# Performance work log

Hardware: AMD Instinct MI355X
Metric: run time of the kernel (lower is better)

Reference implementation:

```python
import jax, jax.numpy as jnp
import numpy as np

# CIM / quantization constants hardcoded in the source module
INPUT_BIT = 8
WEIGHT_BIT = 4
OUTPUT_BIT = 8
DAC_BIT = 2
ADC_BIT = 8
ADC_GAIN_1_SCALE = 1.0 / 63.0
GAIN_MIN, GAIN_MAX = 1.0, 255.0
N_SLICES = INPUT_BIT // DAC_BIT  # 4 bit-serial input slices of 2 bits each


def ste_round(v):
    # straight-through round: forward = round(v), backward = identity
    return v + jax.lax.stop_gradient(jnp.round(v) - v)


def conv2d(x, w):
    # NCHW conv, stride 1, padding k//2 (SAME for odd k)
    return jax.lax.conv_general_dilated(
        x, w, window_strides=(1, 1), padding='SAME',
        dimension_numbers=('NCHW', 'OIHW', 'NCHW'))


def setup_inputs() -> dict:
    key = jax.random.key(0)
    kx, kw, kb = jax.random.split(key, 3)
    B, Cin, H, W = 16, 4, 512, 512
    Cout, K = 8, 3
    x = jax.random.uniform(kx, (B, Cin, H, W), dtype=jnp.float32)  # non-negative activations
    weight = jax.random.normal(kw, (Cout, Cin, K, K), dtype=jnp.float32) * 0.05
    bias = jax.random.normal(kb, (Cout,), dtype=jnp.float32) * 0.01
    s_in = jnp.float32(1.0 / 255.0)   # LSQ input scale (8-bit unsigned)
    s_w = jnp.float32(0.02)           # LSQ weight scale (4-bit signed)
    s_out = jnp.float32(0.05)         # LSQ output scale (8-bit signed)
    return {"x": x, "weight": weight, "bias": bias,
            "s_in": s_in, "s_w": s_w, "s_out": s_out}


def reference(x, weight, bias, s_in, s_w, s_out):
    in_max = 2.0 ** INPUT_BIT - 1.0          # 255
    w_lim = 2.0 ** (WEIGHT_BIT - 1) - 1.0    # 7
    adc_max = 2.0 ** (ADC_BIT - 1) - 1.0     # 127
    o_lim = 2.0 ** (OUTPUT_BIT - 1) - 1.0    # 127
    base = float(2 ** DAC_BIT)               # 4 levels per DAC slice

    # LSQ quantization of input (unsigned) and weight (signed), STE rounding
    xq = jnp.clip(ste_round(x / s_in), 0.0, in_max)        # integer-valued floats
    wq = jnp.clip(ste_round(weight / s_w), -w_lim, w_lim)

    # ideal integer conv (gradient path)
    ideal = conv2d(xq, wq)

    # bit-serial DAC/ADC CIM path (forward only; noise_scale=0 so no noise)
    xi = jax.lax.stop_gradient(xq)
    wi = jax.lax.stop_gradient(wq)
    psums = []
    for s in range(N_SLICES):
        sl = jnp.mod(jnp.floor(xi / (base ** s)), base)    # 2-bit slice in [0,3]
        psums.append(conv2d(sl, wi))
    # ADC gain adjustment ('gain' mode): integer gain in [1,255], LSB = 1/(gain*gain_1_scale)
    p_absmax = jnp.maximum(
        jnp.max(jnp.stack([jnp.max(jnp.abs(p)) for p in psums])), 1e-6)
    gain = jnp.clip(jnp.round(adc_max / (p_absmax * ADC_GAIN_1_SCALE)),
                    GAIN_MIN, GAIN_MAX)
    step = 1.0 / (gain * ADC_GAIN_1_SCALE)
    acc = jnp.zeros_like(ideal)
    for s, p in enumerate(psums):
        adc_out = jnp.clip(jnp.round(p / step), -adc_max, adc_max) * step
        acc = acc + adc_out * (base ** s)

    # straight-through: forward uses analog path, backward uses ideal conv
    psum = ideal + jax.lax.stop_gradient(acc - ideal)

    out = psum * (s_in * s_w) + bias[None, :, None, None]
    # LSQ output quantization (8-bit signed)
    out = jnp.clip(ste_round(out / s_out), -o_lim, o_lim) * s_out
    return out
```

## Files before the change

kernel.cpp:

```cpp
#include <hip/hip_runtime.h>
#include <stdint.h>

#define B_   16
#define CIN  4
#define COUT 8
#define H_   512
#define W_   512
#define HP   (H_ + 2)
#define WP   (W_ + 2)
#define PMAX 756
#define TBL  (2 * PMAX + 1)
#define RPB  8
#define GY   (H_ / RPB)
#define NBLK (2 * GY * B_)
#define NQ   (B_ * HP)

__device__ __forceinline__ int dot4(uint32_t a, int b, int c) {
#if __has_builtin(__builtin_amdgcn_sdot4)
    return __builtin_amdgcn_sdot4((int)a, b, c, false);
#else
    int r = c;
#pragma unroll
    for (int i = 0; i < 4; ++i) {
        int av = (int)((a >> (8 * i)) & 0xFFu);
        int bv = ((int)(((uint32_t)b) << (24 - 8 * i))) >> 24;
        r += av * bv;
    }
    return r;
#endif
}

__device__ __forceinline__ int dot8(uint32_t a, int b, int c) {
#if __has_builtin(__builtin_amdgcn_sdot8)
    return __builtin_amdgcn_sdot8((int)a, b, c, false);
#else
    int r = c;
#pragma unroll
    for (int i = 0; i < 8; ++i) {
        int av = (int)((a >> (4 * i)) & 0xFu);
        int bv = ((int)(((uint32_t)b) << (28 - 4 * i))) >> 28;
        r += av * bv;
    }
    return r;
#endif
}

__device__ __forceinline__ float rfl_f(float v) {
    return __int_as_float(__builtin_amdgcn_readfirstlane(__float_as_int(v)));
}

__device__ __forceinline__ int wquant(const float* w, float s_w,
                                      int co, int ci, int tap) {
    const int kh = tap / 3, kw = tap % 3;
    float wv = w[((co * CIN + ci) * 3 + kh) * 3 + kw];
    float q  = rintf(__fdiv_rn(wv, s_w));
    q = fminf(fmaxf(q, -7.0f), 7.0f);
    return (int)q;
}

__global__ __launch_bounds__(128) void quant_pack_kernel(
        const float* __restrict__ x, const float* __restrict__ weight,
        const float* __restrict__ s_in_p, const float* __restrict__ s_w_p,
        uint32_t* __restrict__ xq, uint32_t* __restrict__ wq8) {
    const int raw = blockIdx.x;
    const int lin = (raw & 7) * (NQ / 8) + (raw >> 3);
    const int b = lin / HP, hp = lin % HP;
    const int t = threadIdx.x;
    if (raw == 0) {
        const float s_w = *s_w_p;
        if (t < 32) {
            const int co = t >> 2, p = t & 3;
            const int tA = (p == 0) ? 0 : (p == 1) ? 3 : (p == 2) ? 6 : 2;
            const int tB = (p == 0) ? 1 : (p == 1) ? 4 : (p == 2) ? 7 : 5;
            uint32_t v = 0;
#pragma unroll
            for (int ci = 0; ci < CIN; ++ci) {
                v |= ((uint32_t)(wquant(weight, s_w, co, ci, tA) & 0xF)) << (8 * ci);
                v |= ((uint32_t)(wquant(weight, s_w, co, ci, tB) & 0xF)) << (8 * ci + 4);
            }
            wq8[t] = v;
        } else if (t < 40) {
            const int co = t - 32;
            uint32_t v = 0;
#pragma unroll
            for (int ci = 0; ci < CIN; ++ci)
                v |= ((uint32_t)(wquant(weight, s_w, co, ci, 8) & 0xFF)) << (8 * ci);
            wq8[32 + co] = v;
        }
    }
    uint32_t* dst = xq + ((size_t)b * HP + hp) * WP;
    if (hp == 0 || hp == HP - 1) {
        for (int i = t; i < WP; i += 128) dst[i] = 0;
        return;
    }
    const float s_in = *s_in_p;
    const int h = hp - 1;
    const size_t plane = (size_t)H_ * W_;
    const float* xr = x + ((size_t)b * CIN) * plane + (size_t)h * W_ + 4 * t;
    float4 v0 = *(const float4*)(xr);
    float4 v1 = *(const float4*)(xr + plane);
    float4 v2 = *(const float4*)(xr + 2 * plane);
    float4 v3 = *(const float4*)(xr + 3 * plane);
    uint32_t o0 = 0, o1 = 0, o2 = 0, o3 = 0;
#define QP(f, ci, oj)                                                  \
    { float q = rintf(__fdiv_rn((f), s_in));                           \
      q = fminf(fmaxf(q, 0.0f), 255.0f);                               \
      oj |= ((uint32_t)(int)q) << (8 * (ci)); }
    QP(v0.x, 0, o0) QP(v0.y, 0, o1) QP(v0.z, 0, o2) QP(v0.w, 0, o3)
    QP(v1.x, 1, o0) QP(v1.y, 1, o1) QP(v1.z, 1, o2) QP(v1.w, 1, o3)
    QP(v2.x, 2, o0) QP(v2.y, 2, o1) QP(v2.z, 2, o2) QP(v2.w, 2, o3)
    QP(v3.x, 3, o0) QP(v3.y, 3, o1) QP(v3.z, 3, o2) QP(v3.w, 3, o3)
#undef QP
    uint32_t* d = dst + 1 + 4 * t;
    d[0] = o0; d[1] = o1; d[2] = o2; d[3] = o3;
    if (t == 0) dst[0] = 0;
    if (t == 127) dst[WP - 1] = 0;
}

#define LOADW()                                                              \
    int w8s[32], w4s[8];                                                     \
    {                                                                        \
        const int4* q4 = (const int4*)wq8;                                   \
        _Pragma("unroll")                                                    \
        for (int i = 0; i < 8; ++i) {                                        \
            int4 w4i = q4[i];                                                \
            w8s[4 * i + 0] = __builtin_amdgcn_readfirstlane(w4i.x);          \
            w8s[4 * i + 1] = __builtin_amdgcn_readfirstlane(w4i.y);          \
            w8s[4 * i + 2] = __builtin_amdgcn_readfirstlane(w4i.z);          \
            w8s[4 * i + 3] = __builtin_amdgcn_readfirstlane(w4i.w);          \
        }                                                                    \
        int4 a0 = q4[8], a1 = q4[9];                                         \
        w4s[0] = __builtin_amdgcn_readfirstlane(a0.x);                       \
        w4s[1] = __builtin_amdgcn_readfirstlane(a0.y);                       \
        w4s[2] = __builtin_amdgcn_readfirstlane(a0.z);                       \
        w4s[3] = __builtin_amdgcn_readfirstlane(a0.w);                       \
        w4s[4] = __builtin_amdgcn_readfirstlane(a1.x);                       \
        w4s[5] = __builtin_amdgcn_readfirstlane(a1.y);                       \
        w4s[6] = __builtin_amdgcn_readfirstlane(a1.z);                       \
        w4s[7] = __builtin_amdgcn_readfirstlane(a1.w);                       \
    }

#define SWZ()                                                                \
    const int raw = blockIdx.x;                                              \
    const int lin = (raw & 7) * (NBLK / 8) + (raw >> 3);                     \
    const int bx = lin & 1;                                                  \
    const int hy = (lin >> 1) & (GY - 1);                                    \
    const int b  = lin >> 7;                                                 \
    const int w0 = bx * 256 + threadIdx.x;                                   \
    const int h0 = hy * RPB;

#define EXTS(CA, SG, v0, v1, v2)                                             \
    do {                                                                     \
        uint32_t lo_ = ((v0) & 0x0F0F0F0Fu) | (((v1) << 4) & 0xF0F0F0F0u);   \
        uint32_t hi_ = (((v0) >> 4) & 0x0F0F0F0Fu) | ((v1) & 0xF0F0F0F0u);   \
        CA[0] = lo_ & 0x33333333u;                                           \
        CA[1] = (lo_ >> 2) & 0x33333333u;                                    \
        CA[2] = hi_ & 0x33333333u;                                           \
        CA[3] = (hi_ >> 2) & 0x33333333u;                                    \
        SG[0] = (v2)&0x03030303u;                                            \
        SG[1] = ((v2) >> 2) & 0x03030303u;                                   \
        SG[2] = ((v2) >> 4) & 0x03030303u;                                   \
        SG[3] = ((v2) >> 6) & 0x03030303u;                                   \
    } while (0)

#define RING_INIT()                                                          \
    uint32_t cA0[4], cA1[4], cA2[4], cA3[4];                                 \
    uint32_t sg0[4], sg1[4], sg2[4], sg3[4];                                 \
    {                                                                        \
        uint32_t r0 = base[0], r1 = base[1], r2 = base[2];                   \
        EXTS(cA0, sg0, r0, r1, r2);                                          \
        r0 = base[WP]; r1 = base[WP + 1]; r2 = base[WP + 2];                 \
        EXTS(cA1, sg1, r0, r1, r2);                                          \
    }                                                                        \
    uint32_t n0 = base[2 * WP], n1 = base[2 * WP + 1], n2 = base[2 * WP + 2];

#define PREF(S)                                                              \
    if ((S) < RPB - 1) {                                                     \
        const uint32_t* nr_ = base + (size_t)((S) + 3) * WP;                 \
        n0 = nr_[0]; n1 = nr_[1]; n2 = nr_[2];                               \
    }

#define DOTS(CAa, SGa, CAb, SGb, CAc, SGc, K, INIT, OUTV)                    \
    {                                                                        \
        int a_ = dot4(SGc[K], w4s[co], INIT);                                \
        a_ = dot8(CAa[K], w8s[co * 4 + 0], a_);                              \
        a_ = dot8(CAb[K], w8s[co * 4 + 1], a_);                              \
        a_ = dot8(CAc[K], w8s[co * 4 + 2], a_);                              \
        a_ = dot8(K == 0 ? pc0 : K == 1 ? pc1 : K == 2 ? pc2 : pc3,          \
                  w8s[co * 4 + 3], a_);                                      \
        OUTV = a_;                                                           \
    }

#define STEP1(S, CAa, SGa, CAb, SGb, CAc, SGc)                               \
    do {                                                                     \
        EXTS(CAc, SGc, n0, n1, n2);                                          \
        PREF(S);                                                             \
        const uint32_t pc0 = SGa[0] | (SGb[0] << 4);                         \
        const uint32_t pc1 = SGa[1] | (SGb[1] << 4);                         \
        const uint32_t pc2 = SGa[2] | (SGb[2] << 4);                         \
        const uint32_t pc3 = SGa[3] | (SGb[3] << 4);                         \
        _Pragma("unroll")                                                    \
        for (int co = 0; co < COUT; ++co) {                                  \
            int a0, a1, a2, a3;                                              \
            DOTS(CAa, SGa, CAb, SGb, CAc, SGc, 0, 0, a0);                    \
            DOTS(CAa, SGa, CAb, SGb, CAc, SGc, 1, 0, a1);                    \
            DOTS(CAa, SGa, CAb, SGb, CAc, SGc, 2, 0, a2);                    \
            DOTS(CAa, SGa, CAb, SGb, CAc, SGc, 3, 0, a3);                    \
            rMax0 = max(rMax0, a0); rMin0 = min(rMin0, a0);                  \
            rMax1 = max(rMax1, a1); rMin1 = min(rMin1, a1);                  \
            rMax2 = max(rMax2, a2); rMin2 = min(rMin2, a2);                  \
            rMax3 = max(rMax3, a3); rMin3 = min(rMin3, a3);                  \
        }                                                                    \
    } while (0)

__global__ __launch_bounds__(256, 8) void conv_absmax(
        const uint32_t* __restrict__ xq, const uint32_t* __restrict__ wq8,
        int* __restrict__ blkmax) {
    __shared__ int red[4];
    LOADW();
    SWZ();
    const uint32_t* base = xq + ((size_t)b * HP + h0) * WP + w0;
    RING_INIT();
    int rMax0 = 0, rMax1 = 0, rMax2 = 0, rMax3 = 0;
    int rMin0 = 0, rMin1 = 0, rMin2 = 0, rMin3 = 0;
    STEP1(0, cA0, sg0, cA1, sg1, cA2, sg2);
    STEP1(1, cA1, sg1, cA2, sg2, cA3, sg3);
    STEP1(2, cA2, sg2, cA3, sg3, cA0, sg0);
    STEP1(3, cA3, sg3, cA0, sg0, cA1, sg1);
    STEP1(4, cA0, sg0, cA1, sg1, cA2, sg2);
    STEP1(5, cA1, sg1, cA2, sg2, cA3, sg3);
    STEP1(6, cA2, sg2, cA3, sg3, cA0, sg0);
    STEP1(7, cA3, sg3, cA0, sg0, cA1, sg1);
    int m = max(max(max(rMax0, -rMin0), max(rMax1, -rMin1)),
                max(max(rMax2, -rMin2), max(rMax3, -rMin3)));
#pragma unroll
    for (int off = 1; off < 64; off <<= 1)
        m = max(m, __shfl_xor(m, off));
    if ((threadIdx.x & 63) == 0) red[threadIdx.x >> 6] = m;
    __syncthreads();
    if (threadIdx.x == 0)
        blkmax[raw] = max(max(red[0], red[1]), max(red[2], red[3]));
}

__global__ __launch_bounds__(256) void reduce_absmax(
        const int* __restrict__ blkmax, int* __restrict__ absmax) {
    __shared__ int red[4];
    const int t = threadIdx.x;
    int m = 0;
#pragma unroll
    for (int i = 0; i < NBLK / 256; ++i) m = max(m, blkmax[t + 256 * i]);
#pragma unroll
    for (int off = 1; off < 64; off <<= 1)
        m = max(m, __shfl_xor(m, off));
    if ((t & 63) == 0) red[t >> 6] = m;
    __syncthreads();
    if (t == 0)
        *absmax = max(max(red[0], red[1]), max(red[2], red[3]));
}

#define STEP2(S, CAa, SGa, CAb, SGb, CAc, SGc)                               \
    do {                                                                     \
        EXTS(CAc, SGc, n0, n1, n2);                                          \
        PREF(S);                                                             \
        const uint32_t pc0 = SGa[0] | (SGb[0] << 4);                         \
        const uint32_t pc1 = SGa[1] | (SGb[1] << 4);                         \
        const uint32_t pc2 = SGa[2] | (SGb[2] << 4);                         \
        const uint32_t pc3 = SGa[3] | (SGb[3] << 4);                         \
        float* orow = out + ((size_t)b * COUT * H_ + (size_t)(h0 + (S))) * W_ + w0; \
        _Pragma("unroll")                                                    \
        for (int co = 0; co < COUT; ++co) {                                  \
            int a0, a1, a2, a3;                                              \
            DOTS(CAa, SGa, CAb, SGb, CAc, SGc, 0, PMAX, a0);                 \
            DOTS(CAa, SGa, CAb, SGb, CAc, SGc, 1, PMAX, a1);                 \
            DOTS(CAa, SGa, CAb, SGb, CAc, SGc, 2, PMAX, a2);                 \
            DOTS(CAa, SGa, CAb, SGb, CAc, SGc, 3, PMAX, a3);                 \
            float of = tbl[a0];                                              \
            of = __fadd_rn(of, __fmul_rn(tbl[a1], 4.0f));                    \
            of = __fadd_rn(of, __fmul_rn(tbl[a2], 16.0f));                   \
            of = __fadd_rn(of, __fmul_rn(tbl[a3], 64.0f));                   \
            float o_ = __fadd_rn(__fmul_rn(of, scale), br[co]);              \
            float q_ = rintf(__fdiv_rn(o_, s_out));                          \
            q_ = fminf(fmaxf(q_, -127.0f), 127.0f);                          \
            orow[(size_t)co * plane] = __fmul_rn(q_, s_out);                 \
        }                                                                    \
    } while (0)

__global__ __launch_bounds__(256, 4) void conv_out(
        const uint32_t* __restrict__ xq, const uint32_t* __restrict__ wq8,
        const float* __restrict__ bias, const float* __restrict__ sp_in,
        const float* __restrict__ sp_w, const float* __restrict__ sp_out,
        const int* __restrict__ absmax, float* __restrict__ out) {
    __shared__ float tbl[TBL];
    LOADW();
    const float pabs = fmaxf((float)(*absmax), 1e-6f);
    const float c63  = 1.0f / 63.0f;
    float g = rintf(__fdiv_rn(127.0f, __fmul_rn(pabs, c63)));
    g = fminf(fmaxf(g, 1.0f), 255.0f);
    const float step = __fdiv_rn(1.0f, __fmul_rn(g, c63));
    for (int i = threadIdx.x; i < TBL; i += 256) {
        float p = (float)(i - PMAX);
        float r = rintf(__fdiv_rn(p, step));
        r = fminf(fmaxf(r, -127.0f), 127.0f);
        tbl[i] = __fmul_rn(r, step);
    }
    const float scale = __fmul_rn(rfl_f(*sp_in), rfl_f(*sp_w));
    const float s_out = rfl_f(*sp_out);
    float br[COUT];
#pragma unroll
    for (int co = 0; co < COUT; ++co) br[co] = rfl_f(bias[co]);
    __syncthreads();

    SWZ();
    const uint32_t* base = xq + ((size_t)b * HP + h0) * WP + w0;
    const size_t plane = (size_t)H_ * W_;
    RING_INIT();
    STEP2(0, cA0, sg0, cA1, sg1, cA2, sg2);
    STEP2(1, cA1, sg1, cA2, sg2, cA3, sg3);
    STEP2(2, cA2, sg2, cA3, sg3, cA0, sg0);
    STEP2(3, cA3, sg3, cA0, sg0, cA1, sg1);
    STEP2(4, cA0, sg0, cA1, sg1, cA2, sg2);
    STEP2(5, cA1, sg1, cA2, sg2, cA3, sg3);
    STEP2(6, cA2, sg2, cA3, sg3, cA0, sg0);
    STEP2(7, cA3, sg3, cA0, sg0, cA1, sg1);
}

extern "C" void kernel_launch(void* const* d_in, const int* in_sizes, int n_in,
                              void* d_out, int out_size, void* d_ws, size_t ws_size,
                              hipStream_t stream) {
    const float* x      = (const float*)d_in[0];
    const float* weight = (const float*)d_in[1];
    const float* bias   = (const float*)d_in[2];
    const float* s_in   = (const float*)d_in[3];
    const float* s_w    = (const float*)d_in[4];
    const float* s_out  = (const float*)d_in[5];
    float* out = (float*)d_out;

    int*      absmax = (int*)d_ws;
    uint32_t* wq8    = (uint32_t*)((char*)d_ws + 256);
    int*      blkmax = (int*)((char*)d_ws + 1024);
    uint32_t* xq     = (uint32_t*)((char*)d_ws + 16384);

    quant_pack_kernel<<<dim3(NQ), dim3(128), 0, stream>>>(
        x, weight, s_in, s_w, xq, wq8);

    conv_absmax<<<dim3(NBLK), dim3(256), 0, stream>>>(xq, wq8, blkmax);

    reduce_absmax<<<dim3(1), dim3(256), 0, stream>>>(blkmax, absmax);

    conv_out<<<dim3(NBLK), dim3(256), 0, stream>>>(
        xq, wq8, bias, s_in, s_w, s_out, absmax, out);
}
```

Baseline: 99.14 us.

## Replace ADC LUT and IEEE divides with reciprocal-based inline quantization

Removes the shared-memory ADC lookup table and its barrier, and computes each ADC quantization inline using a precomputed reciprocal of the step plus one Newton/FMA correction. The IEEE divides in input quantization and output quantization are replaced the same way, which removes the slow division sequences. The launch bound that asked for 4 blocks per SM is dropped, so the compiler has more freedom with registers. The risk is extra ALU work per output in place of LDS gathers, and rounding may differ from exact division in rare ties.

Measured after the change: 111.2 us. 1.12x slower.

```diff
diff --git a/kernel.cpp b/kernel.cpp
--- a/kernel.cpp
+++ b/kernel.cpp
@@ -9,7 +9,6 @@
 #define HP   (H_ + 2)
 #define WP   (W_ + 2)
 #define PMAX 756
-#define TBL  (2 * PMAX + 1)
 #define RPB  8
 #define GY   (H_ / RPB)
 #define NBLK (2 * GY * B_)
@@ -47,6 +46,24 @@
 
 __device__ __forceinline__ float rfl_f(float v) {
     return __int_as_float(__builtin_amdgcn_readfirstlane(__float_as_int(v)));
+}
+
+__device__ __forceinline__ float recip1(float d) {
+    float y0 = __builtin_amdgcn_rcpf(d);
+    float e  = fmaf(-d, y0, 1.0f);
+    return fmaf(y0, e, y0);
+}
+__device__ __forceinline__ float mdiv(float n, float d, float y) {
+    float q0 = __fmul_rn(n, y);
+    float rr = fmaf(-d, q0, n);
+    return fmaf(rr, y, q0);
+}
+
+__device__ __forceinline__ float adc1(int a, float step, float istep) {
+    float pf = (float)a;
+    float q  = rintf(mdiv(pf, step, istep));
+    q = fminf(fmaxf(q, -127.0f), 127.0f);
+    return __fmul_rn(q, step);
 }
 
 __device__ __forceinline__ int wquant(const float* w, float s_w,
@@ -94,6 +111,7 @@
         return;
     }
     const float s_in = *s_in_p;
+    const float yin  = recip1(s_in);
     const int h = hp - 1;
     const size_t plane = (size_t)H_ * W_;
     const float* xr = x + ((size_t)b * CIN) * plane + (size_t)h * W_ + 4 * t;
@@ -103,7 +121,7 @@
     float4 v3 = *(const float4*)(xr + 3 * plane);
     uint32_t o0 = 0, o1 = 0, o2 = 0, o3 = 0;
 #define QP(f, ci, oj)                                                  \
-    { float q = rintf(__fdiv_rn((f), s_in));                           \
+    { float q = rintf(mdiv((f), s_in, yin));                           \
       q = fminf(fmaxf(q, 0.0f), 255.0f);                               \
       oj |= ((uint32_t)(int)q) << (8 * (ci)); }
     QP(v0.x, 0, o0) QP(v0.y, 0, o1) QP(v0.z, 0, o2) QP(v0.w, 0, o3)
@@ -180,9 +198,9 @@
         n0 = nr_[0]; n1 = nr_[1]; n2 = nr_[2];                               \
     }
 
-#define DOTS(CAa, SGa, CAb, SGb, CAc, SGc, K, INIT, OUTV)                    \
+#define DOTS(CAa, SGa, CAb, SGb, CAc, SGc, K, OUTV)                          \
     {                                                                        \
-        int a_ = dot4(SGc[K], w4s[co], INIT);                                \
+        int a_ = dot4(SGc[K], w4s[co], 0);                                   \
         a_ = dot8(CAa[K], w8s[co * 4 + 0], a_);                              \
         a_ = dot8(CAb[K], w8s[co * 4 + 1], a_);                              \
         a_ = dot8(CAc[K], w8s[co * 4 + 2], a_);                              \
@@ -202,10 +220,10 @@
         _Pragma("unroll")                                                    \
         for (int co = 0; co < COUT; ++co) {                                  \
             int a0, a1, a2, a3;                                              \
-            DOTS(CAa, SGa, CAb, SGb, CAc, SGc, 0, 0, a0);                    \
-            DOTS(CAa, SGa, CAb, SGb, CAc, SGc, 1, 0, a1);                    \
-            DOTS(CAa, SGa, CAb, SGb, CAc, SGc, 2, 0, a2);                    \
-            DOTS(CAa, SGa, CAb, SGb, CAc, SGc, 3, 0, a3);                    \
+            DOTS(CAa, SGa, CAb, SGb, CAc, SGc, 0, a0);                       \
+            DOTS(CAa, SGa, CAb, SGb, CAc, SGc, 1, a1);                       \
+            DOTS(CAa, SGa, CAb, SGb, CAc, SGc, 2, a2);                       \
+            DOTS(CAa, SGa, CAb, SGb, CAc, SGc, 3, a3);                       \
             rMax0 = max(rMax0, a0); rMin0 = min(rMin0, a0);                  \
             rMax1 = max(rMax1, a1); rMin1 = min(rMin1, a1);                  \
             rMax2 = max(rMax2, a2); rMin2 = min(rMin2, a2);                  \
@@ -270,45 +288,42 @@
         _Pragma("unroll")                                                    \
         for (int co = 0; co < COUT; ++co) {                                  \
             int a0, a1, a2, a3;                                              \
-            DOTS(CAa, SGa, CAb, SGb, CAc, SGc, 0, PMAX, a0);                 \
-            DOTS(CAa, SGa, CAb, SGb, CAc, SGc, 1, PMAX, a1);                 \
-            DOTS(CAa, SGa, CAb, SGb, CAc, SGc, 2, PMAX, a2);                 \
-            DOTS(CAa, SGa, CAb, SGb, CAc, SGc, 3, PMAX, a3);                 \
-            float of = tbl[a0];                                              \
-            of = __fadd_rn(of, __fmul_rn(tbl[a1], 4.0f));                    \
-            of = __fadd_rn(of, __fmul_rn(tbl[a2], 16.0f));                   \
-            of = __fadd_rn(of, __fmul_rn(tbl[a3], 64.0f));                   \
+            DOTS(CAa, SGa, CAb, SGb, CAc, SGc, 0, a0);                       \
+            DOTS(CAa, SGa, CAb, SGb, CAc, SGc, 1, a1);                       \
+            DOTS(CAa, SGa, CAb, SGb, CAc, SGc, 2, a2);                       \
+            DOTS(CAa, SGa, CAb, SGb, CAc, SGc, 3, a3);                       \
+            float t0 = adc1(a0, step, istep);                                \
+            float t1 = adc1(a1, step, istep);                                \
+            float t2 = adc1(a2, step, istep);                                \
+            float t3 = adc1(a3, step, istep);                                \
+            float of = __fadd_rn(t0, __fmul_rn(t1, 4.0f));                   \
+            of = __fadd_rn(of, __fmul_rn(t2, 16.0f));                       \
+            of = __fadd_rn(of, __fmul_rn(t3, 64.0f));                       \
             float o_ = __fadd_rn(__fmul_rn(of, scale), br[co]);              \
-            float q_ = rintf(__fdiv_rn(o_, s_out));                          \
+            float q_ = rintf(mdiv(o_, s_out, y1));                          \
             q_ = fminf(fmaxf(q_, -127.0f), 127.0f);                          \
             orow[(size_t)co * plane] = __fmul_rn(q_, s_out);                 \
         }                                                                    \
     } while (0)
 
-__global__ __launch_bounds__(256, 4) void conv_out(
+__global__ __launch_bounds__(256) void conv_out(
         const uint32_t* __restrict__ xq, const uint32_t* __restrict__ wq8,
         const float* __restrict__ bias, const float* __restrict__ sp_in,
         const float* __restrict__ sp_w, const float* __restrict__ sp_out,
         const int* __restrict__ absmax, float* __restrict__ out) {
-    __shared__ float tbl[TBL];
     LOADW();
     const float pabs = fmaxf((float)(*absmax), 1e-6f);
     const float c63  = 1.0f / 63.0f;
     float g = rintf(__fdiv_rn(127.0f, __fmul_rn(pabs, c63)));
     g = fminf(fmaxf(g, 1.0f), 255.0f);
-    const float step = __fdiv_rn(1.0f, __fmul_rn(g, c63));
-    for (int i = threadIdx.x; i < TBL; i += 256) {
-        float p = (float)(i - PMAX);
-        float r = rintf(__fdiv_rn(p, step));
-        r = fminf(fmaxf(r, -127.0f), 127.0f);
-        tbl[i] = __fmul_rn(r, step);
-    }
+    const float step  = __fdiv_rn(1.0f, __fmul_rn(g, c63));
+    const float istep = recip1(step);
     const float scale = __fmul_rn(rfl_f(*sp_in), rfl_f(*sp_w));
     const float s_out = rfl_f(*sp_out);
+    const float y1    = recip1(s_out);
     float br[COUT];
 #pragma unroll
     for (int co = 0; co < COUT; ++co) br[co] = rfl_f(bias[co]);
-    __syncthreads();
 
     SWZ();
     const uint32_t* base = xq + ((size_t)b * HP + h0) * WP + w0;
```
